# Kernel optimization log

Hardware: AMD Instinct MI355X
Metric: run time of the kernel (lower is better)

## Reference

```python
import jax, jax.numpy as jnp
import numpy as np

B, C_IN, C_OUT, K, L = 8, 512, 512, 5, 4096
RED = 128  # max(int(512*0.25), 4)
STRIDE, PAD, DIL, GROUPS = 1, 2, 1, 1


def setup_inputs() -> dict:
    key = jax.random.key(0)
    ks = jax.random.split(key, 20)

    def n(k, shape, scale=0.05):
        return jax.random.normal(k, shape, jnp.float32) * scale

    inp = {
        "x": jax.random.normal(ks[0], (B, C_IN, L), jnp.float32),
        "weight": n(ks[1], (C_OUT, C_IN // GROUPS, K), 0.05),
        "bias": jnp.zeros((C_OUT,), jnp.float32),
    }
    # four attention branches: avgpool -> 1x1 conv (C_in->RED) -> relu -> 1x1 conv (RED->out) -> sigmoid
    for i, (nm, od) in enumerate(zip(["ka", "sa", "ia", "oa"], [K, 1, C_IN, C_OUT])):
        inp[nm + "_w1"] = n(ks[2 + 4 * i], (RED, C_IN))
        inp[nm + "_b1"] = jnp.zeros((RED,), jnp.float32)
        inp[nm + "_w2"] = n(ks[3 + 4 * i], (od, RED))
        inp[nm + "_b2"] = jnp.zeros((od,), jnp.float32)
    return inp


def _att(avg, w1, b1, w2, b2):
    # avg: [B, C_in]; two 1x1 convs over a length-1 signal == two dense layers
    h = jax.nn.relu(avg @ w1.T + b1)
    return jax.nn.sigmoid(h @ w2.T + b2)


def reference(x, weight, bias,
              ka_w1, ka_b1, ka_w2, ka_b2,
              sa_w1, sa_b1, sa_w2, sa_b2,
              ia_w1, ia_b1, ia_w2, ia_b2,
              oa_w1, oa_b1, oa_w2, oa_b2):
    b, c, l = x.shape
    avg = x.mean(axis=2)                     # AdaptiveAvgPool1d(1) -> [B, C_in]
    ka = _att(avg, ka_w1, ka_b1, ka_w2, ka_b2)  # [B, K]
    sa = _att(avg, sa_w1, sa_b1, sa_w2, sa_b2)  # [B, 1]
    ia = _att(avg, ia_w1, ia_b1, ia_w2, ia_b2)  # [B, C_in]
    oa = _att(avg, oa_w1, oa_b1, oa_w2, oa_b2)  # [B, C_out]
    # dynamic weight [B, C_out, C_in//g, K]; note ia broadcasts on the OUT-channel
    # axis (faithful to the torch broadcasting, which requires C_in == C_out)
    dw = (weight[None]
          * ka[:, None, None, :]
          * sa[:, :, None, None]
          * ia[:, :, None, None]
          * oa[:, :, None, None])
    dw = dw.reshape(b * C_OUT, C_IN // GROUPS, K)
    xg = x.reshape(1, b * c, l)
    out = jax.lax.conv_general_dilated(
        xg, dw,
        window_strides=(STRIDE,),
        padding=[(PAD, PAD)],
        rhs_dilation=(DIL,),
        feature_group_count=b * GROUPS,
        dimension_numbers=("NCH", "OIH", "NCH"))
    out = out.reshape(b, C_OUT, -1) + bias[None, :, None]
    return out
```

## Files before the change

### kernel.cpp

```cpp
#include <hip/hip_runtime.h>

typedef unsigned short u16;
typedef __bf16 bf16x8 __attribute__((ext_vector_type(8)));
typedef float f32x4 __attribute__((ext_vector_type(4)));
typedef u16 u16x8 __attribute__((ext_vector_type(8)));

#define B_    8
#define CIN   512
#define COUT  512
#define KT    5
#define LEN   4096
#define RED_  128
#define KDIM  (KT * CIN)
#define BSR   40

__device__ __forceinline__ u16 f2bf(float f) {
    unsigned int u = __float_as_uint(f);
    u += 0x7fffu + ((u >> 16) & 1u);
    return (u16)(u >> 16);
}

typedef __attribute__((address_space(1))) void gvoid_t;
typedef __attribute__((address_space(3))) void lvoid_t;
__device__ __forceinline__ void glds16(const u16* g, u16* l) {
    __builtin_amdgcn_global_load_lds((gvoid_t*)g, (lvoid_t*)l, 16, 0, 0);
}

__global__ void avg_kernel(const float* __restrict__ x, float* __restrict__ avg) {
    const int row = blockIdx.x;
    const float4* xr = (const float4*)(x + (size_t)row * LEN);
    float sum = 0.f;
    for (int j = threadIdx.x; j < LEN / 4; j += 256) {
        float4 v = xr[j];
        sum += v.x + v.y + v.z + v.w;
    }
#pragma unroll
    for (int off = 32; off > 0; off >>= 1) sum += __shfl_down(sum, off, 64);
    __shared__ float red[4];
    if ((threadIdx.x & 63) == 0) red[threadIdx.x >> 6] = sum;
    __syncthreads();
    if (threadIdx.x == 0)
        avg[row] = (red[0] + red[1] + red[2] + red[3]) * (1.0f / LEN);
}

__global__ void attn_kernel(const float* __restrict__ avg,
    const float* kw1, const float* kb1, const float* kw2, const float* kb2,
    const float* sw1, const float* sb1, const float* sw2, const float* sb2,
    const float* iw1, const float* ib1, const float* iw2, const float* ib2,
    const float* ow1, const float* ob1, const float* ow2, const float* ob2,
    float* __restrict__ ka, float* __restrict__ sa,
    float* __restrict__ ia, float* __restrict__ oa) {
    const int br = blockIdx.x >> 3, b = blockIdx.x & 7;
    const float *w1, *b1p, *w2, *b2p; float* op; int od;
    if (br == 0)      { w1 = kw1; b1p = kb1; w2 = kw2; b2p = kb2; op = ka + b * KT;  od = KT;   }
    else if (br == 1) { w1 = sw1; b1p = sb1; w2 = sw2; b2p = sb2; op = sa + b;       od = 1;    }
    else if (br == 2) { w1 = iw1; b1p = ib1; w2 = iw2; b2p = ib2; op = ia + b * CIN; od = CIN;  }
    else              { w1 = ow1; b1p = ob1; w2 = ow2; b2p = ob2; op = oa + b * COUT; od = COUT; }

    __shared__ float av[CIN];
    __shared__ float h[RED_];
    const int t = threadIdx.x;
    for (int j = t; j < CIN; j += RED_) av[j] = avg[b * CIN + j];
    __syncthreads();
    float acc = b1p[t];
    const float4* wr = (const float4*)(w1 + (size_t)t * CIN);
#pragma unroll 4
    for (int c = 0; c < CIN / 4; ++c) {
        float4 w = wr[c];
        acc += av[4 * c] * w.x + av[4 * c + 1] * w.y + av[4 * c + 2] * w.z + av[4 * c + 3] * w.w;
    }
    h[t] = fmaxf(acc, 0.f);
    __syncthreads();
    for (int o = t; o < od; o += RED_) {
        float a2 = b2p[o];
        const float4* w2r = (const float4*)(w2 + (size_t)o * RED_);
#pragma unroll 4
        for (int j = 0; j < RED_ / 4; ++j) {
            float4 w = w2r[j];
            a2 += h[4 * j] * w.x + h[4 * j + 1] * w.y + h[4 * j + 2] * w.z + h[4 * j + 3] * w.w;
        }
        op[o] = 1.f / (1.f + expf(-a2));
    }
}

__global__ void scomb_kernel(const float* __restrict__ sa, const float* __restrict__ ia,
                             const float* __restrict__ oa, float* __restrict__ s) {
    int idx = blockIdx.x * 256 + threadIdx.x;
    int b = idx >> 9;
    s[idx] = sa[b] * ia[idx] * oa[idx];
}

__global__ void wbgen_kernel(const float* __restrict__ w, const float* __restrict__ ka,
                             u16* __restrict__ wb) {
    int u = blockIdx.x * 256 + threadIdx.x;
    int i8 = (u & 63) << 3;
    int t = u >> 6;
    int k = t % KT;
    int o = (t / KT) & 511;
    int b = t / (KT * 512);
    float kav = ka[b * KT + k];
    const float* wp = w + ((size_t)o * CIN + i8) * KT + k;
    u16x8 r;
#pragma unroll
    for (int j = 0; j < 8; ++j) r[j] = f2bf(wp[(size_t)j * KT] * kav);
    *(u16x8*)(wb + ((size_t)(b * COUT + o)) * KDIM + k * CIN + i8) = r;
}

__global__ __launch_bounds__(256) void gemm_kernel(
    const u16* __restrict__ wb, const float* __restrict__ x,
    const float* __restrict__ s, const float* __restrict__ bias,
    float* __restrict__ out) {
    __shared__ __align__(16) u16 As[5 * 128 * 32];
    __shared__ __align__(16) u16 Bs[132 * BSR];
    __shared__ float sm[128], bm[128];

    const int l0 = blockIdx.x * 128;
    const int o0 = blockIdx.y * 128;
    const int b  = blockIdx.z;
    const int tid = threadIdx.x;

    if (tid < 128) {
        sm[tid] = s[b * COUT + o0 + tid];
        bm[tid] = bias[o0 + tid];
    }

    const int lane = tid & 63;
    const int wave = tid >> 6;
    const int wm = (wave >> 1) * 64;
    const int wn = (wave & 1) * 64;
    const int lm = lane & 15;
    const int quad = lane >> 4;

    f32x4 acc[4][4];
#pragma unroll
    for (int i = 0; i < 4; ++i)
#pragma unroll
        for (int j = 0; j < 4; ++j) {
            f32x4 zz = {0.f, 0.f, 0.f, 0.f};
            acc[i][j] = zz;
        }

    const float* xb = x + (size_t)b * CIN * LEN;
    const u16* gA = wb + ((size_t)(b * COUT + o0 + (tid >> 2))) * KDIM + (tid & 3) * 8;
    const int lwA = tid & 63;
    const int igA = (tid >> 6) * 8;

#pragma unroll 1
    for (int ic = 0; ic < 16; ++ic) {
        const int i0 = ic * 32;
#pragma unroll
        for (int t = 0; t < KT; ++t) {
            glds16(gA + t * 512 + i0, &As[t * 4096 + tid * 8]);
            glds16(gA + (size_t)64 * KDIM + t * 512 + i0, &As[t * 4096 + 2048 + tid * 8]);
        }
#pragma unroll
        for (int rg = 0; rg < 2; ++rg) {
            const int lw = lwA + rg * 64;
            const int lg = l0 - 2 + lw;
            if (lg >= 0 && lg < LEN) {
                const float* xp = xb + (size_t)(i0 + igA) * LEN + lg;
                unsigned d0, d1, d2, d3;
                {
                    unsigned a = __float_as_uint(xp[0]);
                    unsigned c = __float_as_uint(xp[(size_t)LEN]);
                    d0 = __builtin_amdgcn_perm(c, a, 0x07060302);
                    a = __float_as_uint(xp[(size_t)2 * LEN]);
                    c = __float_as_uint(xp[(size_t)3 * LEN]);
                    d1 = __builtin_amdgcn_perm(c, a, 0x07060302);
                    a = __float_as_uint(xp[(size_t)4 * LEN]);
                    c = __float_as_uint(xp[(size_t)5 * LEN]);
                    d2 = __builtin_amdgcn_perm(c, a, 0x07060302);
                    a = __float_as_uint(xp[(size_t)6 * LEN]);
                    c = __float_as_uint(xp[(size_t)7 * LEN]);
                    d3 = __builtin_amdgcn_perm(c, a, 0x07060302);
                }
                *(uint4*)&Bs[lw * BSR + igA] = make_uint4(d0, d1, d2, d3);
            } else {
                *(uint4*)&Bs[lw * BSR + igA] = make_uint4(0, 0, 0, 0);
            }
        }
        if (tid < 16) {
            const int lw = 128 + (tid >> 2);
            const int ig = (tid & 3) * 8;
            const int lg = l0 - 2 + lw;
            if (lg >= 0 && lg < LEN) {
                const float* xp = xb + (size_t)(i0 + ig) * LEN + lg;
                unsigned d[4];
#pragma unroll
                for (int jj = 0; jj < 4; ++jj) {
                    unsigned a = __float_as_uint(xp[(size_t)(2 * jj) * LEN]);
                    unsigned c = __float_as_uint(xp[(size_t)(2 * jj + 1) * LEN]);
                    d[jj] = __builtin_amdgcn_perm(c, a, 0x07060302);
                }
                *(uint4*)&Bs[lw * BSR + ig] = make_uint4(d[0], d[1], d[2], d[3]);
            } else {
                *(uint4*)&Bs[lw * BSR + ig] = make_uint4(0, 0, 0, 0);
            }
        }
        __syncthreads();

#pragma unroll
        for (int t = 0; t < KT; ++t) {
            bf16x8 af[4], bfr[4];
#pragma unroll
            for (int f = 0; f < 4; ++f) {
                af[f]  = *(const bf16x8*)&As[t * 4096 + (wm + f * 16 + lm) * 32 + quad * 8];
                bfr[f] = *(const bf16x8*)&Bs[(wn + f * 16 + lm + t) * BSR + quad * 8];
            }
#pragma unroll
            for (int mt = 0; mt < 4; ++mt)
#pragma unroll
                for (int nt = 0; nt < 4; ++nt)
                    acc[mt][nt] = __builtin_amdgcn_mfma_f32_16x16x32_bf16(
                        af[mt], bfr[nt], acc[mt][nt], 0, 0, 0);
        }
        __syncthreads();
    }

#pragma unroll
    for (int mt = 0; mt < 4; ++mt) {
        const int mb = wm + mt * 16 + quad * 4;
        float sv[4], bv[4];
#pragma unroll
        for (int r = 0; r < 4; ++r) { sv[r] = sm[mb + r]; bv[r] = bm[mb + r]; }
#pragma unroll
        for (int nt = 0; nt < 4; ++nt) {
            const int col = l0 + wn + nt * 16 + lm;
            float* op = out + ((size_t)(b * COUT + o0 + mb)) * LEN + col;
#pragma unroll
            for (int r = 0; r < 4; ++r)
                op[(size_t)r * LEN] = sv[r] * acc[mt][nt][r] + bv[r];
        }
    }
}

extern "C" void kernel_launch(void* const* d_in, const int* in_sizes, int n_in,
                              void* d_out, int out_size, void* d_ws, size_t ws_size,
                              hipStream_t stream) {
    const float* x      = (const float*)d_in[0];
    const float* weight = (const float*)d_in[1];
    const float* bias   = (const float*)d_in[2];
    float* out = (float*)d_out;

    char* ws = (char*)d_ws;
    size_t off = 0;
    auto alloc = [&](size_t bytes) {
        void* p = ws + off;
        off += (bytes + 255) & ~(size_t)255;
        return p;
    };
    u16*   wbuf = (u16*)alloc((size_t)B_ * COUT * KDIM * sizeof(u16));
    float* avg  = (float*)alloc((size_t)B_ * CIN * sizeof(float));
    float* ka   = (float*)alloc((size_t)B_ * KT * sizeof(float));
    float* sa   = (float*)alloc((size_t)B_ * sizeof(float));
    float* ia   = (float*)alloc((size_t)B_ * CIN * sizeof(float));
    float* oa   = (float*)alloc((size_t)B_ * COUT * sizeof(float));
    float* sfac = (float*)alloc((size_t)B_ * COUT * sizeof(float));

    avg_kernel<<<B_ * CIN, 256, 0, stream>>>(x, avg);
    attn_kernel<<<32, RED_, 0, stream>>>(avg,
        (const float*)d_in[3],  (const float*)d_in[4],  (const float*)d_in[5],  (const float*)d_in[6],
        (const float*)d_in[7],  (const float*)d_in[8],  (const float*)d_in[9],  (const float*)d_in[10],
        (const float*)d_in[11], (const float*)d_in[12], (const float*)d_in[13], (const float*)d_in[14],
        (const float*)d_in[15], (const float*)d_in[16], (const float*)d_in[17], (const float*)d_in[18],
        ka, sa, ia, oa);
    scomb_kernel<<<(B_ * COUT) / 256, 256, 0, stream>>>(sa, ia, oa, sfac);
    wbgen_kernel<<<(B_ * COUT * KT * 64) / 256, 256, 0, stream>>>(weight, ka, wbuf);
    gemm_kernel<<<dim3(LEN / 128, COUT / 128, B_), 256, 0, stream>>>(
        wbuf, x, sfac, bias, out);
}
```

Measured before the change: 301.1 us.

## Load GEMM weights directly to registers, restage wbgen via LDS, fuse scale combine

The GEMM no longer stages the A (weight) tile in LDS with global_load_lds. Each lane now loads its MFMA A fragments straight from global memory, prefetching the next k-slice while the current one runs, which frees the LDS and allows a launch bound of 3 blocks. The wbgen kernel now reads each output channel's weight row into shared memory once and writes the bf16 rows for all batches from there, instead of doing strided global reads. The scomb kernel is folded into the GEMM prologue, and attn is reorganised around wave-level reductions over 256 threads. Direct global A loads are reused across 4 column waves only through cache, which may add global traffic and latency.

```diff
diff --git a/kernel.cpp b/kernel.cpp
--- a/kernel.cpp
+++ b/kernel.cpp
@@ -18,12 +18,6 @@
     unsigned int u = __float_as_uint(f);
     u += 0x7fffu + ((u >> 16) & 1u);
     return (u16)(u >> 16);
-}
-
-typedef __attribute__((address_space(1))) void gvoid_t;
-typedef __attribute__((address_space(3))) void lvoid_t;
-__device__ __forceinline__ void glds16(const u16* g, u16* l) {
-    __builtin_amdgcn_global_load_lds((gvoid_t*)g, (lvoid_t*)l, 16, 0, 0);
 }
 
 __global__ void avg_kernel(const float* __restrict__ x, float* __restrict__ avg) {
@@ -57,24 +51,28 @@
     else if (br == 2) { w1 = iw1; b1p = ib1; w2 = iw2; b2p = ib2; op = ia + b * CIN; od = CIN;  }
     else              { w1 = ow1; b1p = ob1; w2 = ow2; b2p = ob2; op = oa + b * COUT; od = COUT; }
 
-    __shared__ float av[CIN];
+    const int t = threadIdx.x;
+    const int lane = t & 63, wv = t >> 6;
     __shared__ float h[RED_];
-    const int t = threadIdx.x;
-    for (int j = t; j < CIN; j += RED_) av[j] = avg[b * CIN + j];
+
+    const float4 av0 = *(const float4*)(avg + b * CIN + lane * 8);
+    const float4 av1 = *(const float4*)(avg + b * CIN + lane * 8 + 4);
+
+    for (int r = wv * 32; r < wv * 32 + 32; ++r) {
+        const float4* wr = (const float4*)(w1 + (size_t)r * CIN + lane * 8);
+        float4 x0 = wr[0], x1 = wr[1];
+        float sacc = x0.x * av0.x + x0.y * av0.y + x0.z * av0.z + x0.w * av0.w
+                   + x1.x * av1.x + x1.y * av1.y + x1.z * av1.z + x1.w * av1.w;
+#pragma unroll
+        for (int off = 32; off > 0; off >>= 1) sacc += __shfl_down(sacc, off, 64);
+        if (lane == 0) h[r] = fmaxf(sacc + b1p[r], 0.f);
+    }
     __syncthreads();
-    float acc = b1p[t];
-    const float4* wr = (const float4*)(w1 + (size_t)t * CIN);
-#pragma unroll 4
-    for (int c = 0; c < CIN / 4; ++c) {
-        float4 w = wr[c];
-        acc += av[4 * c] * w.x + av[4 * c + 1] * w.y + av[4 * c + 2] * w.z + av[4 * c + 3] * w.w;
-    }
-    h[t] = fmaxf(acc, 0.f);
-    __syncthreads();
-    for (int o = t; o < od; o += RED_) {
+
+    for (int o = t; o < od; o += 256) {
         float a2 = b2p[o];
         const float4* w2r = (const float4*)(w2 + (size_t)o * RED_);
-#pragma unroll 4
+#pragma unroll 8
         for (int j = 0; j < RED_ / 4; ++j) {
             float4 w = w2r[j];
             a2 += h[4 * j] * w.x + h[4 * j + 1] * w.y + h[4 * j + 2] * w.z + h[4 * j + 3] * w.w;
@@ -83,34 +81,36 @@
     }
 }
 
-__global__ void scomb_kernel(const float* __restrict__ sa, const float* __restrict__ ia,
-                             const float* __restrict__ oa, float* __restrict__ s) {
-    int idx = blockIdx.x * 256 + threadIdx.x;
-    int b = idx >> 9;
-    s[idx] = sa[b] * ia[idx] * oa[idx];
-}
-
-__global__ void wbgen_kernel(const float* __restrict__ w, const float* __restrict__ ka,
-                             u16* __restrict__ wb) {
-    int u = blockIdx.x * 256 + threadIdx.x;
-    int i8 = (u & 63) << 3;
-    int t = u >> 6;
-    int k = t % KT;
-    int o = (t / KT) & 511;
-    int b = t / (KT * 512);
-    float kav = ka[b * KT + k];
-    const float* wp = w + ((size_t)o * CIN + i8) * KT + k;
-    u16x8 r;
-#pragma unroll
-    for (int j = 0; j < 8; ++j) r[j] = f2bf(wp[(size_t)j * KT] * kav);
-    *(u16x8*)(wb + ((size_t)(b * COUT + o)) * KDIM + k * CIN + i8) = r;
-}
-
-__global__ __launch_bounds__(256) void gemm_kernel(
+__global__ __launch_bounds__(256) void wbgen_kernel(const float* __restrict__ w,
+                                                    const float* __restrict__ ka,
+                                                    u16* __restrict__ wb) {
+    __shared__ float wt[KDIM];
+    const int o = blockIdx.x;
+    const int tid = threadIdx.x;
+    const float4* wr = (const float4*)(w + (size_t)o * KDIM);
+    for (int j = tid; j < KDIM / 4; j += 256)
+        *(float4*)&wt[4 * j] = wr[j];
+    __syncthreads();
+    for (int b = 0; b < B_; ++b) {
+        u16* wrow = wb + ((size_t)(b * COUT + o)) * KDIM;
+        for (int e8 = tid * 8; e8 < KDIM; e8 += 2048) {
+            const int k = e8 >> 9;
+            const int ib = e8 & 511;
+            const float kav = ka[b * KT + k];
+            u16x8 r;
+#pragma unroll
+            for (int j = 0; j < 8; ++j)
+                r[j] = f2bf(wt[(ib + j) * KT + k] * kav);
+            *(u16x8*)(wrow + e8) = r;
+        }
+    }
+}
+
+__global__ __launch_bounds__(256, 3) void gemm_kernel(
     const u16* __restrict__ wb, const float* __restrict__ x,
-    const float* __restrict__ s, const float* __restrict__ bias,
+    const float* __restrict__ sa, const float* __restrict__ ia,
+    const float* __restrict__ oa, const float* __restrict__ bias,
     float* __restrict__ out) {
-    __shared__ __align__(16) u16 As[5 * 128 * 32];
     __shared__ __align__(16) u16 Bs[132 * BSR];
     __shared__ float sm[128], bm[128];
 
@@ -120,8 +120,9 @@
     const int tid = threadIdx.x;
 
     if (tid < 128) {
-        sm[tid] = s[b * COUT + o0 + tid];
-        bm[tid] = bias[o0 + tid];
+        const int o = o0 + tid;
+        sm[tid] = sa[b] * ia[b * CIN + o] * oa[b * COUT + o];
+        bm[tid] = bias[o];
     }
 
     const int lane = tid & 63;
@@ -141,18 +142,18 @@
         }
 
     const float* xb = x + (size_t)b * CIN * LEN;
-    const u16* gA = wb + ((size_t)(b * COUT + o0 + (tid >> 2))) * KDIM + (tid & 3) * 8;
+    const u16* gA = wb + ((size_t)(b * COUT + o0 + wm + lm)) * KDIM + quad * 8;
     const int lwA = tid & 63;
     const int igA = (tid >> 6) * 8;
+
+    bf16x8 afc[4], afn[4];
+#pragma unroll
+    for (int f = 0; f < 4; ++f)
+        afc[f] = *(const bf16x8*)(gA + (size_t)(f * 16) * KDIM);
 
 #pragma unroll 1
     for (int ic = 0; ic < 16; ++ic) {
         const int i0 = ic * 32;
-#pragma unroll
-        for (int t = 0; t < KT; ++t) {
-            glds16(gA + t * 512 + i0, &As[t * 4096 + tid * 8]);
-            glds16(gA + (size_t)64 * KDIM + t * 512 + i0, &As[t * 4096 + 2048 + tid * 8]);
-        }
 #pragma unroll
         for (int rg = 0; rg < 2; ++rg) {
             const int lw = lwA + rg * 64;
@@ -201,18 +202,22 @@
 
 #pragma unroll
         for (int t = 0; t < KT; ++t) {
-            bf16x8 af[4], bfr[4];
-#pragma unroll
-            for (int f = 0; f < 4; ++f) {
-                af[f]  = *(const bf16x8*)&As[t * 4096 + (wm + f * 16 + lm) * 32 + quad * 8];
+            const int noff = (t < 4) ? (t + 1) * 512 + i0 : i0 + 32;
+#pragma unroll
+            for (int f = 0; f < 4; ++f)
+                afn[f] = *(const bf16x8*)(gA + (size_t)(f * 16) * KDIM + noff);
+            bf16x8 bfr[4];
+#pragma unroll
+            for (int f = 0; f < 4; ++f)
                 bfr[f] = *(const bf16x8*)&Bs[(wn + f * 16 + lm + t) * BSR + quad * 8];
-            }
 #pragma unroll
             for (int mt = 0; mt < 4; ++mt)
 #pragma unroll
                 for (int nt = 0; nt < 4; ++nt)
                     acc[mt][nt] = __builtin_amdgcn_mfma_f32_16x16x32_bf16(
-                        af[mt], bfr[nt], acc[mt][nt], 0, 0, 0);
+                        afc[mt], bfr[nt], acc[mt][nt], 0, 0, 0);
+#pragma unroll
+            for (int f = 0; f < 4; ++f) afc[f] = afn[f];
         }
         __syncthreads();
     }
@@ -255,17 +260,15 @@
     float* sa   = (float*)alloc((size_t)B_ * sizeof(float));
     float* ia   = (float*)alloc((size_t)B_ * CIN * sizeof(float));
     float* oa   = (float*)alloc((size_t)B_ * COUT * sizeof(float));
-    float* sfac = (float*)alloc((size_t)B_ * COUT * sizeof(float));
 
     avg_kernel<<<B_ * CIN, 256, 0, stream>>>(x, avg);
-    attn_kernel<<<32, RED_, 0, stream>>>(avg,
+    attn_kernel<<<32, 256, 0, stream>>>(avg,
         (const float*)d_in[3],  (const float*)d_in[4],  (const float*)d_in[5],  (const float*)d_in[6],
         (const float*)d_in[7],  (const float*)d_in[8],  (const float*)d_in[9],  (const float*)d_in[10],
         (const float*)d_in[11], (const float*)d_in[12], (const float*)d_in[13], (const float*)d_in[14],
         (const float*)d_in[15], (const float*)d_in[16], (const float*)d_in[17], (const float*)d_in[18],
         ka, sa, ia, oa);
-    scomb_kernel<<<(B_ * COUT) / 256, 256, 0, stream>>>(sa, ia, oa, sfac);
-    wbgen_kernel<<<(B_ * COUT * KT * 64) / 256, 256, 0, stream>>>(weight, ka, wbuf);
+    wbgen_kernel<<<COUT, 256, 0, stream>>>(weight, ka, wbuf);
     gemm_kernel<<<dim3(LEN / 128, COUT / 128, B_), 256, 0, stream>>>(
-        wbuf, x, sfac, bias, out);
-}
+        wbuf, x, sa, ia, oa, bias, out);
+}
```

New measurement: 345.4 us. 1.15x slower.
